# Kernel tuning notes

Hardware: AMD Instinct MI355X
Metric: run time of the kernel (lower is better)

## Reference

```python
import jax, jax.numpy as jnp
import numpy as np

D_IN, L, D, K, N_CLASSES = 1024, 512, 384, 1, 2

def setup_inputs() -> dict:
    key = jax.random.key(0)
    ks = jax.random.split(key, 11)
    x = jax.random.normal(ks[0], (2, 40000, D_IN), dtype=jnp.float32)
    # Linear params stored as [in, out]; xavier-normal-ish scale
    def w(k, i, o):
        return jax.random.normal(k, (i, o), dtype=jnp.float32) * jnp.sqrt(2.0 / (i + o))
    return {
        "x": x,
        "Wf": w(ks[1], D_IN, L), "bf": jnp.zeros((L,), jnp.float32),
        "Wa": w(ks[2], L, D),    "ba": jnp.zeros((D,), jnp.float32),
        "Wb": w(ks[3], L, D),    "bb": jnp.zeros((D,), jnp.float32),
        "Wc": w(ks[4], D, K),    "bc": jnp.zeros((K,), jnp.float32),
        "Wcls": w(ks[5], L * K, N_CLASSES), "bcls": jnp.zeros((N_CLASSES,), jnp.float32),
    }

def reference(x, Wf, bf, Wa, ba, Wb, bb, Wc, bc, Wcls, bcls):
    # feature embed: Linear + ReLU  (mil_norm=None -> Identity norms)
    h = jax.nn.relu(jnp.einsum('bnd,de->bne', x, Wf) + bf)   # [B,N,L]
    # gated attention
    a = jnp.tanh(jnp.einsum('bnl,ld->bnd', h, Wa) + ba)      # [B,N,D]
    g = jax.nn.sigmoid(jnp.einsum('bnl,ld->bnd', h, Wb) + bb)
    s = jnp.einsum('bnd,dk->bnk', a * g, Wc) + bc            # [B,N,K]
    A = jax.nn.softmax(jnp.swapaxes(s, -1, -2), axis=-1)     # [B,K,N]
    pooled = jnp.einsum('bkn,bnl->bkl', A, h)                # [B,K,L]
    logits = jnp.squeeze(pooled, 1) @ Wcls + bcls            # [B,n_classes]
    return logits
```

## Files before the change

### kernel.cpp

```cpp
#include <hip/hip_runtime.h>
#include <cstdint>

typedef _Float16 f16;
typedef __attribute__((ext_vector_type(8))) _Float16 half8;
typedef __attribute__((ext_vector_type(2))) _Float16 half2v;
typedef __attribute__((ext_vector_type(4))) float floatx4;

#define M_TOTAL 80000
#define NB      40000
#define DIN     1024
#define LDIM    512
#define DDIM    384

__global__ void k_prep(const float* __restrict__ Wf, const float* __restrict__ Wa,
                       const float* __restrict__ Wb,
                       f16* __restrict__ WfT, f16* __restrict__ WaT, f16* __restrict__ WbT)
{
    const int gid = blockIdx.x * 256 + threadIdx.x;
    if (gid < 512 * 1024) {
        const int n = gid >> 10, k = gid & 1023;
        WfT[gid] = (f16)Wf[k * 512 + n];
    } else if (gid < 512 * 1024 + 384 * 512) {
        const int g = gid - 512 * 1024;
        const int n = g >> 9, k = g & 511;
        WaT[g] = (f16)Wa[k * 384 + n];
    } else if (gid < 512 * 1024 + 2 * 384 * 512) {
        const int g = gid - 512 * 1024 - 384 * 512;
        const int n = g >> 9, k = g & 511;
        WbT[g] = (f16)Wb[k * 384 + n];
    }
}

__global__ __launch_bounds__(256, 2) void k_gemm1(
    const float* __restrict__ x, const f16* __restrict__ WfT,
    const float* __restrict__ bf, f16* __restrict__ h)
{
    __shared__ __align__(16) f16 As[64 * 40];
    __shared__ __align__(16) f16 Bs[512 * 40];
    const int tid  = threadIdx.x;
    const int wave = tid >> 6;
    const int lane = tid & 63;
    const int lr   = lane & 15;
    const int lq   = lane >> 4;
    const long row0 = (long)blockIdx.x * 64;

    floatx4 acc[4][8] = {};

    const int ra = tid >> 2;
    const int ka = (tid & 3) * 8;
    const float* xrow = x + (row0 + ra) * DIN + ka;

    for (int kt = 0; kt < DIN / 32; ++kt) {
        const int k0 = kt * 32;
        __syncthreads();
        {
            const float4* p = (const float4*)(xrow + k0);
            float4 f0 = p[0];
            float4 f1 = p[1];
            half8 hv;
            hv[0] = (f16)f0.x; hv[1] = (f16)f0.y; hv[2] = (f16)f0.z; hv[3] = (f16)f0.w;
            hv[4] = (f16)f1.x; hv[5] = (f16)f1.y; hv[6] = (f16)f1.z; hv[7] = (f16)f1.w;
            *(half8*)&As[ra * 40 + ka] = hv;
        }
        #pragma unroll
        for (int rnd = 0; rnd < 8; ++rnd) {
            const int n = (tid >> 2) + rnd * 64;
            *(half8*)&Bs[n * 40 + ka] = *(const half8*)&WfT[(long)n * DIN + k0 + ka];
        }
        __syncthreads();
        half8 af[4];
        #pragma unroll
        for (int ti = 0; ti < 4; ++ti)
            af[ti] = *(const half8*)&As[(ti * 16 + lr) * 40 + lq * 8];
        #pragma unroll
        for (int tj = 0; tj < 8; ++tj) {
            half8 bfrag = *(const half8*)&Bs[(wave * 128 + tj * 16 + lr) * 40 + lq * 8];
            #pragma unroll
            for (int ti = 0; ti < 4; ++ti)
                acc[ti][tj] = __builtin_amdgcn_mfma_f32_16x16x32_f16(af[ti], bfrag, acc[ti][tj], 0, 0, 0);
        }
    }
    #pragma unroll
    for (int tj = 0; tj < 8; ++tj) {
        const int col = wave * 128 + tj * 16 + lr;
        const float bias = bf[col];
        #pragma unroll
        for (int ti = 0; ti < 4; ++ti) {
            const long rg = row0 + ti * 16 + lq * 4;
            #pragma unroll
            for (int r = 0; r < 4; ++r) {
                float v = acc[ti][tj][r] + bias;
                v = fmaxf(v, 0.0f);
                h[(rg + r) * LDIM + col] = (f16)v;
            }
        }
    }
}

__device__ inline float fast_sigmoid(float xx) { return 1.0f / (1.0f + __expf(-xx)); }
__device__ inline float fast_tanh(float xx) {
    float e = __expf(-2.0f * fabsf(xx));
    float r = (1.0f - e) / (1.0f + e);
    return xx >= 0.0f ? r : -r;
}

__global__ __launch_bounds__(256, 2) void k_gemm2(
    const f16* __restrict__ h, const f16* __restrict__ WaT, const f16* __restrict__ WbT,
    const float* __restrict__ ba, const float* __restrict__ bb,
    const float* __restrict__ Wc, float* __restrict__ s)
{
    __shared__ __align__(16) f16 Hs [128 * 72];
    __shared__ __align__(16) f16 Bas[128 * 72];
    __shared__ __align__(16) f16 Bbs[128 * 72];
    const int tid = threadIdx.x;
    const int bx  = blockIdx.x;
    const int rb  = bx / 3;
    const int cc  = bx - rb * 3;
    const long row0 = (long)rb * 128;
    const int col0  = cc * 128;
    const int wave = tid >> 6, lane = tid & 63;
    const int wr = wave >> 1, wc = wave & 1;
    const int lr = lane & 15, lq = lane >> 4;

    floatx4 aacc[4][4] = {};
    floatx4 gacc[4][4] = {};

    for (int kt = 0; kt < 8; ++kt) {
        const int k0 = kt * 64;
        __syncthreads();
        #pragma unroll
        for (int rnd = 0; rnd < 4; ++rnd) {
            const int j  = rnd * 256 + tid;
            const int rr = j >> 3;
            const int kq = (j & 7) * 8;
            *(half8*)&Hs [rr * 72 + kq] = *(const half8*)&h  [(row0 + rr) * LDIM + k0 + kq];
            *(half8*)&Bas[rr * 72 + kq] = *(const half8*)&WaT[(long)(col0 + rr) * LDIM + k0 + kq];
            *(half8*)&Bbs[rr * 72 + kq] = *(const half8*)&WbT[(long)(col0 + rr) * LDIM + k0 + kq];
        }
        __syncthreads();
        #pragma unroll
        for (int kk = 0; kk < 2; ++kk) {
            const int kb = kk * 32 + lq * 8;
            half8 af[4];
            #pragma unroll
            for (int ti = 0; ti < 4; ++ti)
                af[ti] = *(const half8*)&Hs[(wr * 64 + ti * 16 + lr) * 72 + kb];
            #pragma unroll
            for (int tj = 0; tj < 4; ++tj) {
                half8 b1 = *(const half8*)&Bas[(wc * 64 + tj * 16 + lr) * 72 + kb];
                #pragma unroll
                for (int ti = 0; ti < 4; ++ti)
                    aacc[ti][tj] = __builtin_amdgcn_mfma_f32_16x16x32_f16(af[ti], b1, aacc[ti][tj], 0, 0, 0);
            }
            #pragma unroll
            for (int tj = 0; tj < 4; ++tj) {
                half8 b2 = *(const half8*)&Bbs[(wc * 64 + tj * 16 + lr) * 72 + kb];
                #pragma unroll
                for (int ti = 0; ti < 4; ++ti)
                    gacc[ti][tj] = __builtin_amdgcn_mfma_f32_16x16x32_f16(af[ti], b2, gacc[ti][tj], 0, 0, 0);
            }
        }
    }
    float sp[4][4] = {};
    #pragma unroll
    for (int tj = 0; tj < 4; ++tj) {
        const int colg = col0 + wc * 64 + tj * 16 + lr;
        const float biasA = ba[colg];
        const float biasB = bb[colg];
        const float wcv   = Wc[colg];
        #pragma unroll
        for (int ti = 0; ti < 4; ++ti)
            #pragma unroll
            for (int r = 0; r < 4; ++r) {
                const float av = fast_tanh(aacc[ti][tj][r] + biasA);
                const float gv = fast_sigmoid(gacc[ti][tj][r] + biasB);
                sp[ti][r] += av * gv * wcv;
            }
    }
    #pragma unroll
    for (int m = 1; m < 16; m <<= 1)
        #pragma unroll
        for (int ti = 0; ti < 4; ++ti)
            #pragma unroll
            for (int r = 0; r < 4; ++r)
                sp[ti][r] += __shfl_xor(sp[ti][r], m, 64);
    if (lr == 0) {
        #pragma unroll
        for (int ti = 0; ti < 4; ++ti)
            #pragma unroll
            for (int r = 0; r < 4; ++r)
                atomicAdd(&s[row0 + wr * 64 + ti * 16 + lq * 4 + r], sp[ti][r]);
    }
}

__global__ void k_stats(const float* __restrict__ s, float* __restrict__ stats)
{
    const int b = blockIdx.x;
    const int tid = threadIdx.x;
    const float* sb = s + b * NB;
    __shared__ float red[4];
    __shared__ float red2[4];
    __shared__ float smax_sh;
    float m = -3.4e38f;
    for (int i = tid; i < NB; i += 256) m = fmaxf(m, sb[i]);
    #pragma unroll
    for (int o = 32; o > 0; o >>= 1) m = fmaxf(m, __shfl_xor(m, o, 64));
    if ((tid & 63) == 0) red[tid >> 6] = m;
    __syncthreads();
    if (tid == 0) smax_sh = fmaxf(fmaxf(red[0], red[1]), fmaxf(red[2], red[3]));
    __syncthreads();
    const float smax = smax_sh;
    float sum = 0.0f;
    for (int i = tid; i < NB; i += 256) sum += __expf(sb[i] - smax);
    #pragma unroll
    for (int o = 32; o > 0; o >>= 1) sum += __shfl_xor(sum, o, 64);
    if ((tid & 63) == 0) red2[tid >> 6] = sum;
    __syncthreads();
    if (tid == 0) {
        stats[b * 2]     = smax;
        stats[b * 2 + 1] = red2[0] + red2[1] + red2[2] + red2[3];
    }
}

__global__ __launch_bounds__(256) void k_pool(
    const f16* __restrict__ h, const float* __restrict__ s,
    const float* __restrict__ stats, float* __restrict__ pooled)
{
    const int bx = blockIdx.x;
    const int b  = bx / 200;
    const int ch = bx - b * 200;
    const float smax = stats[b * 2];
    const long nbase = (long)b * NB + (long)ch * 200;
    const int c0 = threadIdx.x * 2;
    float a0 = 0.0f, a1 = 0.0f;
    for (int r = 0; r < 200; ++r) {
        const long n = nbase + r;
        const float w = __expf(s[n] - smax);
        half2v hv = *(const half2v*)&h[n * LDIM + c0];
        a0 += w * (float)hv[0];
        a1 += w * (float)hv[1];
    }
    atomicAdd(&pooled[b * LDIM + c0], a0);
    atomicAdd(&pooled[b * LDIM + c0 + 1], a1);
}

__global__ void k_logits(const float* __restrict__ pooled, const float* __restrict__ stats,
                         const float* __restrict__ Wcls, const float* __restrict__ bcls,
                         float* __restrict__ out)
{
    const int tid = threadIdx.x;
    const int wave = tid >> 6, lane = tid & 63;
    const int b = wave >> 1, c = wave & 1;
    float sum = 0.0f;
    for (int l = lane; l < LDIM; l += 64)
        sum += pooled[b * LDIM + l] * Wcls[l * 2 + c];
    #pragma unroll
    for (int o = 32; o > 0; o >>= 1) sum += __shfl_xor(sum, o, 64);
    if (lane == 0) out[b * 2 + c] = sum / stats[b * 2 + 1] + bcls[c];
}

extern "C" void kernel_launch(void* const* d_in, const int* in_sizes, int n_in,
                              void* d_out, int out_size, void* d_ws, size_t ws_size,
                              hipStream_t stream)
{
    const float* x    = (const float*)d_in[0];
    const float* Wf   = (const float*)d_in[1];
    const float* bf   = (const float*)d_in[2];
    const float* Wa   = (const float*)d_in[3];
    const float* ba   = (const float*)d_in[4];
    const float* Wb   = (const float*)d_in[5];
    const float* bb   = (const float*)d_in[6];
    const float* Wc   = (const float*)d_in[7];
    const float* Wcls = (const float*)d_in[9];
    const float* bcls = (const float*)d_in[10];
    float* out = (float*)d_out;

    char* w = (char*)d_ws;
    f16*   WfT    = (f16*)(w);
    f16*   WaT    = (f16*)(w + 1048576);
    f16*   WbT    = (f16*)(w + 1441792);
    f16*   hbuf   = (f16*)(w + 1835008);
    float* sbuf   = (float*)(w + 83755008);
    float* stats  = (float*)(w + 84075008);
    float* pooled = (float*)(w + 84075136);

    hipMemsetAsync(sbuf, 0, 320000, stream);
    hipMemsetAsync(pooled, 0, 4096, stream);

    k_prep  <<<3584, 256, 0, stream>>>(Wf, Wa, Wb, WfT, WaT, WbT);
    k_gemm1 <<<M_TOTAL / 64, 256, 0, stream>>>(x, WfT, bf, hbuf);
    k_gemm2 <<<(M_TOTAL / 128) * 3, 256, 0, stream>>>(hbuf, WaT, WbT, ba, bb, Wc, sbuf);
    k_stats <<<2, 256, 0, stream>>>(sbuf, stats);
    k_pool  <<<400, 256, 0, stream>>>(hbuf, sbuf, stats, pooled);
    k_logits<<<1, 256, 0, stream>>>(pooled, stats, Wcls, bcls, out);
}
```

Baseline: 718.5 us.

## Pre-pack weights in MFMA fragment order and load B operands directly from global

Weights are repacked into MFMA-fragment-ordered fp16 buffers so both GEMMs read B fragments straight from global/L2 instead of staging them through shared memory. The Wa and Wb columns are interleaved into one packed buffer. GEMM2 now covers all 384 output columns per 64-row block, so h is read once per block instead of three times, and the tanh/sigmoid pairs sit in the same thread. Both GEMMs use 512-thread blocks with double-buffered activation tiles and register prefetch. The pooling kernel uses 8-wide fp16 loads plus a shared-memory reduction before the atomics. The trade-off is heavier per-wave global traffic for weights, which depends on L2 hits, and higher register pressure.

Measured after the change: 824.7 us. 1.15x slower.

```diff
diff --git a/kernel.cpp b/kernel.cpp
--- a/kernel.cpp
+++ b/kernel.cpp
@@ -3,95 +3,106 @@
 
 typedef _Float16 f16;
 typedef __attribute__((ext_vector_type(8))) _Float16 half8;
-typedef __attribute__((ext_vector_type(2))) _Float16 half2v;
 typedef __attribute__((ext_vector_type(4))) float floatx4;
 
+#define NB      40000
 #define M_TOTAL 80000
-#define NB      40000
 #define DIN     1024
 #define LDIM    512
 #define DDIM    384
 
 __global__ void k_prep(const float* __restrict__ Wf, const float* __restrict__ Wa,
                        const float* __restrict__ Wb,
-                       f16* __restrict__ WfT, f16* __restrict__ WaT, f16* __restrict__ WbT)
+                       f16* __restrict__ packedF, f16* __restrict__ packedAB)
 {
     const int gid = blockIdx.x * 256 + threadIdx.x;
-    if (gid < 512 * 1024) {
-        const int n = gid >> 10, k = gid & 1023;
-        WfT[gid] = (f16)Wf[k * 512 + n];
-    } else if (gid < 512 * 1024 + 384 * 512) {
-        const int g = gid - 512 * 1024;
-        const int n = g >> 9, k = g & 511;
-        WaT[g] = (f16)Wa[k * 384 + n];
-    } else if (gid < 512 * 1024 + 2 * 384 * 512) {
-        const int g = gid - 512 * 1024 - 384 * 512;
-        const int n = g >> 9, k = g & 511;
-        WbT[g] = (f16)Wb[k * 384 + n];
-    }
-}
-
-__global__ __launch_bounds__(256, 2) void k_gemm1(
-    const float* __restrict__ x, const f16* __restrict__ WfT,
+    if (gid < 65536) {
+        const int lq = gid & 3, n = (gid >> 2) & 511, kb = gid >> 11;
+        const int kbase = kb * 32 + lq * 8;
+        half8 v;
+        #pragma unroll
+        for (int j = 0; j < 8; ++j) v[j] = (f16)Wf[(kbase + j) * 512 + n];
+        *(half8*)&packedF[(long)gid * 8] = v;
+    } else if (gid < 65536 + 49152) {
+        const int g = gid - 65536;
+        const int kb = g / 3072;
+        const int rem = g - kb * 3072;
+        const int c = rem >> 2, lq = rem & 3;
+        const int d = ((c >> 5) << 4) + (c & 15);
+        const int type = (c >> 4) & 1;
+        const float* src = type ? Wb : Wa;
+        const int kbase = kb * 32 + lq * 8;
+        half8 v;
+        #pragma unroll
+        for (int j = 0; j < 8; ++j) v[j] = (f16)src[(kbase + j) * 384 + d];
+        *(half8*)&packedAB[(long)g * 8] = v;
+    }
+}
+
+__global__ __launch_bounds__(512, 4) void k_gemm1(
+    const float* __restrict__ x, const f16* __restrict__ packedF,
     const float* __restrict__ bf, f16* __restrict__ h)
 {
-    __shared__ __align__(16) f16 As[64 * 40];
-    __shared__ __align__(16) f16 Bs[512 * 40];
-    const int tid  = threadIdx.x;
-    const int wave = tid >> 6;
-    const int lane = tid & 63;
-    const int lr   = lane & 15;
-    const int lq   = lane >> 4;
+    __shared__ __align__(16) f16 As[2][64][72];
+    const int tid = threadIdx.x;
+    const int w = tid >> 6, lane = tid & 63, lr = lane & 15, lq = lane >> 4;
     const long row0 = (long)blockIdx.x * 64;
-
-    floatx4 acc[4][8] = {};
-
-    const int ra = tid >> 2;
-    const int ka = (tid & 3) * 8;
-    const float* xrow = x + (row0 + ra) * DIN + ka;
-
-    for (int kt = 0; kt < DIN / 32; ++kt) {
-        const int k0 = kt * 32;
+    const int sr = tid >> 3, sk = (tid & 7) * 8;
+    const float* xp = x + (row0 + sr) * DIN + sk;
+
+    floatx4 acc[4][4] = {};
+
+    float4 xa = *(const float4*)xp;
+    float4 xb = *(const float4*)(xp + 4);
+    {
+        half8 hv;
+        hv[0]=(f16)xa.x; hv[1]=(f16)xa.y; hv[2]=(f16)xa.z; hv[3]=(f16)xa.w;
+        hv[4]=(f16)xb.x; hv[5]=(f16)xb.y; hv[6]=(f16)xb.z; hv[7]=(f16)xb.w;
+        *(half8*)&As[0][sr][sk] = hv;
+    }
+    for (int kt = 0; kt < 16; ++kt) {
         __syncthreads();
-        {
-            const float4* p = (const float4*)(xrow + k0);
-            float4 f0 = p[0];
-            float4 f1 = p[1];
+        const int cur = kt & 1;
+        if (kt < 15) {
+            const float* q = xp + (kt + 1) * 64;
+            xa = *(const float4*)q;
+            xb = *(const float4*)(q + 4);
+        }
+        #pragma unroll
+        for (int kq = 0; kq < 2; ++kq) {
+            const int kb = kt * 2 + kq;
+            half8 bfr[4];
+            #pragma unroll
+            for (int tj = 0; tj < 4; ++tj)
+                bfr[tj] = *(const half8*)&packedF[(long)((kb * 512 + w * 64 + tj * 16 + lr) << 5) + lq * 8];
+            half8 af[4];
+            #pragma unroll
+            for (int ti = 0; ti < 4; ++ti)
+                af[ti] = *(const half8*)&As[cur][ti * 16 + lr][kq * 32 + lq * 8];
+            #pragma unroll
+            for (int tj = 0; tj < 4; ++tj)
+                #pragma unroll
+                for (int ti = 0; ti < 4; ++ti)
+                    acc[ti][tj] = __builtin_amdgcn_mfma_f32_16x16x32_f16(af[ti], bfr[tj], acc[ti][tj], 0, 0, 0);
+        }
+        if (kt < 15) {
             half8 hv;
-            hv[0] = (f16)f0.x; hv[1] = (f16)f0.y; hv[2] = (f16)f0.z; hv[3] = (f16)f0.w;
-            hv[4] = (f16)f1.x; hv[5] = (f16)f1.y; hv[6] = (f16)f1.z; hv[7] = (f16)f1.w;
-            *(half8*)&As[ra * 40 + ka] = hv;
-        }
-        #pragma unroll
-        for (int rnd = 0; rnd < 8; ++rnd) {
-            const int n = (tid >> 2) + rnd * 64;
-            *(half8*)&Bs[n * 40 + ka] = *(const half8*)&WfT[(long)n * DIN + k0 + ka];
-        }
-        __syncthreads();
-        half8 af[4];
-        #pragma unroll
-        for (int ti = 0; ti < 4; ++ti)
-            af[ti] = *(const half8*)&As[(ti * 16 + lr) * 40 + lq * 8];
-        #pragma unroll
-        for (int tj = 0; tj < 8; ++tj) {
-            half8 bfrag = *(const half8*)&Bs[(wave * 128 + tj * 16 + lr) * 40 + lq * 8];
-            #pragma unroll
-            for (int ti = 0; ti < 4; ++ti)
-                acc[ti][tj] = __builtin_amdgcn_mfma_f32_16x16x32_f16(af[ti], bfrag, acc[ti][tj], 0, 0, 0);
-        }
-    }
-    #pragma unroll
-    for (int tj = 0; tj < 8; ++tj) {
-        const int col = wave * 128 + tj * 16 + lr;
+            hv[0]=(f16)xa.x; hv[1]=(f16)xa.y; hv[2]=(f16)xa.z; hv[3]=(f16)xa.w;
+            hv[4]=(f16)xb.x; hv[5]=(f16)xb.y; hv[6]=(f16)xb.z; hv[7]=(f16)xb.w;
+            *(half8*)&As[cur ^ 1][sr][sk] = hv;
+        }
+    }
+    #pragma unroll
+    for (int tj = 0; tj < 4; ++tj) {
+        const int col = w * 64 + tj * 16 + lr;
         const float bias = bf[col];
         #pragma unroll
         for (int ti = 0; ti < 4; ++ti) {
-            const long rg = row0 + ti * 16 + lq * 4;
+            const long rbase = row0 + ti * 16 + lq * 4;
             #pragma unroll
             for (int r = 0; r < 4; ++r) {
-                float v = acc[ti][tj][r] + bias;
-                v = fmaxf(v, 0.0f);
-                h[(rg + r) * LDIM + col] = (f16)v;
+                float v = fmaxf(acc[ti][tj][r] + bias, 0.0f);
+                h[(rbase + r) * LDIM + col] = (f16)v;
             }
         }
     }
@@ -104,76 +115,64 @@
     return xx >= 0.0f ? r : -r;
 }
 
-__global__ __launch_bounds__(256, 2) void k_gemm2(
-    const f16* __restrict__ h, const f16* __restrict__ WaT, const f16* __restrict__ WbT,
+__global__ __launch_bounds__(512, 2) void k_gemm2(
+    const f16* __restrict__ h, const f16* __restrict__ packedAB,
     const float* __restrict__ ba, const float* __restrict__ bb,
     const float* __restrict__ Wc, float* __restrict__ s)
 {
-    __shared__ __align__(16) f16 Hs [128 * 72];
-    __shared__ __align__(16) f16 Bas[128 * 72];
-    __shared__ __align__(16) f16 Bbs[128 * 72];
-    const int tid = threadIdx.x;
-    const int bx  = blockIdx.x;
-    const int rb  = bx / 3;
-    const int cc  = bx - rb * 3;
-    const long row0 = (long)rb * 128;
-    const int col0  = cc * 128;
-    const int wave = tid >> 6, lane = tid & 63;
-    const int wr = wave >> 1, wc = wave & 1;
-    const int lr = lane & 15, lq = lane >> 4;
-
-    floatx4 aacc[4][4] = {};
-    floatx4 gacc[4][4] = {};
-
-    for (int kt = 0; kt < 8; ++kt) {
-        const int k0 = kt * 64;
+    __shared__ __align__(16) f16 Hs[2][64][136];
+    const int tid = threadIdx.x;
+    const int w = tid >> 6, lane = tid & 63, lr = lane & 15, lq = lane >> 4;
+    const long row0 = (long)blockIdx.x * 64;
+    const int sr = tid >> 3, sk = (tid & 7) * 16;
+    const f16* hp = h + (row0 + sr) * LDIM + sk;
+
+    floatx4 acc[4][6] = {};
+
+    half8 s0 = *(const half8*)hp;
+    half8 s1 = *(const half8*)(hp + 8);
+    *(half8*)&Hs[0][sr][sk]     = s0;
+    *(half8*)&Hs[0][sr][sk + 8] = s1;
+
+    for (int kt = 0; kt < 4; ++kt) {
         __syncthreads();
-        #pragma unroll
-        for (int rnd = 0; rnd < 4; ++rnd) {
-            const int j  = rnd * 256 + tid;
-            const int rr = j >> 3;
-            const int kq = (j & 7) * 8;
-            *(half8*)&Hs [rr * 72 + kq] = *(const half8*)&h  [(row0 + rr) * LDIM + k0 + kq];
-            *(half8*)&Bas[rr * 72 + kq] = *(const half8*)&WaT[(long)(col0 + rr) * LDIM + k0 + kq];
-            *(half8*)&Bbs[rr * 72 + kq] = *(const half8*)&WbT[(long)(col0 + rr) * LDIM + k0 + kq];
-        }
-        __syncthreads();
-        #pragma unroll
-        for (int kk = 0; kk < 2; ++kk) {
-            const int kb = kk * 32 + lq * 8;
+        const int cur = kt & 1;
+        if (kt < 3) {
+            const f16* q = hp + (kt + 1) * 128;
+            s0 = *(const half8*)q;
+            s1 = *(const half8*)(q + 8);
+        }
+        #pragma unroll
+        for (int kq = 0; kq < 4; ++kq) {
+            const int kb = kt * 4 + kq;
             half8 af[4];
             #pragma unroll
             for (int ti = 0; ti < 4; ++ti)
-                af[ti] = *(const half8*)&Hs[(wr * 64 + ti * 16 + lr) * 72 + kb];
-            #pragma unroll
-            for (int tj = 0; tj < 4; ++tj) {
-                half8 b1 = *(const half8*)&Bas[(wc * 64 + tj * 16 + lr) * 72 + kb];
+                af[ti] = *(const half8*)&Hs[cur][ti * 16 + lr][kq * 32 + lq * 8];
+            #pragma unroll
+            for (int tj = 0; tj < 6; ++tj) {
+                half8 bfr = *(const half8*)&packedAB[(long)((kb * 768 + w * 96 + tj * 16 + lr) << 5) + lq * 8];
                 #pragma unroll
                 for (int ti = 0; ti < 4; ++ti)
-                    aacc[ti][tj] = __builtin_amdgcn_mfma_f32_16x16x32_f16(af[ti], b1, aacc[ti][tj], 0, 0, 0);
+                    acc[ti][tj] = __builtin_amdgcn_mfma_f32_16x16x32_f16(af[ti], bfr, acc[ti][tj], 0, 0, 0);
             }
-            #pragma unroll
-            for (int tj = 0; tj < 4; ++tj) {
-                half8 b2 = *(const half8*)&Bbs[(wc * 64 + tj * 16 + lr) * 72 + kb];
-                #pragma unroll
-                for (int ti = 0; ti < 4; ++ti)
-                    gacc[ti][tj] = __builtin_amdgcn_mfma_f32_16x16x32_f16(af[ti], b2, gacc[ti][tj], 0, 0, 0);
-            }
+        }
+        if (kt < 3) {
+            *(half8*)&Hs[cur ^ 1][sr][sk]     = s0;
+            *(half8*)&Hs[cur ^ 1][sr][sk + 8] = s1;
         }
     }
     float sp[4][4] = {};
     #pragma unroll
-    for (int tj = 0; tj < 4; ++tj) {
-        const int colg = col0 + wc * 64 + tj * 16 + lr;
-        const float biasA = ba[colg];
-        const float biasB = bb[colg];
-        const float wcv   = Wc[colg];
+    for (int u = 0; u < 3; ++u) {
+        const int d = w * 48 + u * 16 + lr;
+        const float biasA = ba[d], biasB = bb[d], wcv = Wc[d];
         #pragma unroll
         for (int ti = 0; ti < 4; ++ti)
             #pragma unroll
             for (int r = 0; r < 4; ++r) {
-                const float av = fast_tanh(aacc[ti][tj][r] + biasA);
-                const float gv = fast_sigmoid(gacc[ti][tj][r] + biasB);
+                const float av = fast_tanh(acc[ti][2 * u][r] + biasA);
+                const float gv = fast_sigmoid(acc[ti][2 * u + 1][r] + biasB);
                 sp[ti][r] += av * gv * wcv;
             }
     }
@@ -189,7 +188,7 @@
         for (int ti = 0; ti < 4; ++ti)
             #pragma unroll
             for (int r = 0; r < 4; ++r)
-                atomicAdd(&s[row0 + wr * 64 + ti * 16 + lq * 4 + r], sp[ti][r]);
+                atomicAdd(&s[row0 + ti * 16 + lq * 4 + r], sp[ti][r]);
     }
 }
 
@@ -226,22 +225,31 @@
     const f16* __restrict__ h, const float* __restrict__ s,
     const float* __restrict__ stats, float* __restrict__ pooled)
 {
+    __shared__ float red[4][512];
     const int bx = blockIdx.x;
-    const int b  = bx / 200;
-    const int ch = bx - b * 200;
+    const int b = bx / 250, ch = bx - b * 250;
     const float smax = stats[b * 2];
-    const long nbase = (long)b * NB + (long)ch * 200;
-    const int c0 = threadIdx.x * 2;
-    float a0 = 0.0f, a1 = 0.0f;
-    for (int r = 0; r < 200; ++r) {
+    const int tid = threadIdx.x;
+    const int rg = tid >> 6, cl = (tid & 63) * 8;
+    const long nbase = (long)b * NB + ch * 160;
+    float a[8] = {};
+    for (int r = rg; r < 160; r += 4) {
         const long n = nbase + r;
-        const float w = __expf(s[n] - smax);
-        half2v hv = *(const half2v*)&h[n * LDIM + c0];
-        a0 += w * (float)hv[0];
-        a1 += w * (float)hv[1];
-    }
-    atomicAdd(&pooled[b * LDIM + c0], a0);
-    atomicAdd(&pooled[b * LDIM + c0 + 1], a1);
+        const float wgt = __expf(s[n] - smax);
+        half8 hv = *(const half8*)&h[n * LDIM + cl];
+        #pragma unroll
+        for (int j = 0; j < 8; ++j) a[j] += wgt * (float)hv[j];
+    }
+    #pragma unroll
+    for (int j = 0; j < 8; ++j) red[rg][cl + j] = a[j];
+    __syncthreads();
+    if (rg == 0) {
+        #pragma unroll
+        for (int j = 0; j < 8; ++j) {
+            const int c = cl + j;
+            atomicAdd(&pooled[b * LDIM + c], red[0][c] + red[1][c] + red[2][c] + red[3][c]);
+        }
+    }
 }
 
 __global__ void k_logits(const float* __restrict__ pooled, const float* __restrict__ stats,
@@ -276,21 +284,20 @@
     float* out = (float*)d_out;
 
     char* w = (char*)d_ws;
-    f16*   WfT    = (f16*)(w);
-    f16*   WaT    = (f16*)(w + 1048576);
-    f16*   WbT    = (f16*)(w + 1441792);
-    f16*   hbuf   = (f16*)(w + 1835008);
-    float* sbuf   = (float*)(w + 83755008);
-    float* stats  = (float*)(w + 84075008);
-    float* pooled = (float*)(w + 84075136);
+    f16*   packedF  = (f16*)(w);
+    f16*   packedAB = (f16*)(w + 1048576);
+    f16*   hbuf     = (f16*)(w + 1835008);
+    float* sbuf     = (float*)(w + 83755008);
+    float* stats    = (float*)(w + 84075008);
+    float* pooled   = (float*)(w + 84075136);
 
     hipMemsetAsync(sbuf, 0, 320000, stream);
     hipMemsetAsync(pooled, 0, 4096, stream);
 
-    k_prep  <<<3584, 256, 0, stream>>>(Wf, Wa, Wb, WfT, WaT, WbT);
-    k_gemm1 <<<M_TOTAL / 64, 256, 0, stream>>>(x, WfT, bf, hbuf);
-    k_gemm2 <<<(M_TOTAL / 128) * 3, 256, 0, stream>>>(hbuf, WaT, WbT, ba, bb, Wc, sbuf);
+    k_prep  <<<448, 256, 0, stream>>>(Wf, Wa, Wb, packedF, packedAB);
+    k_gemm1 <<<M_TOTAL / 64, 512, 0, stream>>>(x, packedF, bf, hbuf);
+    k_gemm2 <<<M_TOTAL / 64, 512, 0, stream>>>(hbuf, packedAB, ba, bb, Wc, sbuf);
     k_stats <<<2, 256, 0, stream>>>(sbuf, stats);
-    k_pool  <<<400, 256, 0, stream>>>(hbuf, sbuf, stats, pooled);
+    k_pool  <<<500, 256, 0, stream>>>(hbuf, sbuf, stats, pooled);
     k_logits<<<1, 256, 0, stream>>>(pooled, stats, Wcls, bcls, out);
 }
```
